# Kernel tuning notes

Measured on AMD Instinct MI355X. Metric: run time of the kernel, lower is better.

The kernel has to match this reference:

```python
import jax, jax.numpy as jnp
import numpy as np

NUM_EMBEDDINGS = 1024
EMBEDDING_DIM = 256
COMMITMENT_COST = 0.25


def setup_inputs() -> dict:
    key = jax.random.key(0)
    k1, k2 = jax.random.split(key)
    x = jax.random.normal(k1, (16, 4096, EMBEDDING_DIM), dtype=jnp.float32)
    init_bound = 1.0 / NUM_EMBEDDINGS
    embedding = jax.random.uniform(
        k2, (NUM_EMBEDDINGS, EMBEDDING_DIM), dtype=jnp.float32,
        minval=-init_bound, maxval=init_bound)
    return {"x": x, "embedding": embedding}


def reference(x, embedding):
    # dim = -1, so no moveaxis needed; flatten all leading dims.
    E = embedding.shape[1]
    N = embedding.shape[0]
    x_flat = jax.lax.stop_gradient(x).reshape(-1, E)            # [M, E]
    M = x_flat.shape[0]

    distances = (
        jnp.sum(x_flat * x_flat, axis=1, keepdims=True)          # [M, 1]
        + jnp.sum(embedding * embedding, axis=1)                  # [N]
        - 2.0 * (x_flat @ embedding.T)                            # [M, N]
    )
    idx = jnp.argmin(distances, axis=1)                           # [M]
    quantized = embedding[idx].reshape(x.shape)                   # gather

    # losses (non-EMA branch)
    e_latent_loss = jnp.mean((jax.lax.stop_gradient(quantized) - x) ** 2)
    q_latent_loss = jnp.mean((quantized - jax.lax.stop_gradient(x)) ** 2)
    loss = q_latent_loss + COMMITMENT_COST * e_latent_loss

    # straight-through estimator
    quantized_st = x + jax.lax.stop_gradient(quantized - x)

    # perplexity: mean of one-hot == normalized code-usage histogram
    counts = jnp.zeros((N,), jnp.float32).at[idx].add(1.0)
    avg_probs = counts / M
    perplexity = jnp.exp(-jnp.sum(avg_probs * jnp.log(avg_probs + 1e-10)))

    return quantized_st, loss, perplexity
```

## Files before the change

### kernel.cpp

```cpp
#include <hip/hip_runtime.h>


#define VQ_M 65536
#define VQ_N 1024
#define VQ_E 256

typedef __attribute__((ext_vector_type(8))) short bf16x8;
typedef __attribute__((ext_vector_type(4))) float f32x4;

__device__ __forceinline__ ushort f2b(float f) {
  unsigned u = __float_as_uint(f);
  unsigned r = (u + 0x7FFFu + ((u >> 16) & 1u)) >> 16;
  return (ushort)r;
}

__global__ __launch_bounds__(256) void vq_prep(
    const float* __restrict__ emb, float* __restrict__ en2h,
    ushort* __restrict__ embB, unsigned* __restrict__ counts,
    double* __restrict__ loss_sum) {
  const int tid  = threadIdx.x;
  const int lane = tid & 63;
  const int n    = blockIdx.x * 4 + (tid >> 6);
  const float4 e4 = reinterpret_cast<const float4*>(emb)[n * 64 + lane];
  double s = (double)e4.x * e4.x + (double)e4.y * e4.y +
             (double)e4.z * e4.z + (double)e4.w * e4.w;
#pragma unroll
  for (int m = 1; m < 64; m <<= 1) s += __shfl_xor(s, m, 64);
  if (lane == 0) en2h[n] = (float)(-0.5 * s);
  ushort4 b;
  b.x = f2b(e4.x); b.y = f2b(e4.y); b.z = f2b(e4.z); b.w = f2b(e4.w);
  reinterpret_cast<ushort4*>(embB)[n * 64 + lane] = b;
  if (blockIdx.x == 0) {
#pragma unroll
    for (int j = 0; j < 4; ++j) counts[tid + j * 256] = 0u;
    if (tid == 0) *loss_sum = 0.0;
  }
}

__global__ __launch_bounds__(256, 2) void vq_argmin_mfma(
    const float* __restrict__ X, const ushort* __restrict__ embB,
    const float* __restrict__ en2h, int* __restrict__ idxOut) {
  __shared__ ushort lds[2][64 * 256];
  const int tid = threadIdx.x;
  const int w   = tid >> 6;
  const int l   = tid & 63;
  const int lr  = l & 15;
  const int g4  = l >> 4;
  const int m0  = blockIdx.x * 128;

  bf16x8 xf[2][8];
#pragma unroll
  for (int fx = 0; fx < 2; ++fx)
#pragma unroll
    for (int kc = 0; kc < 8; ++kc) {
      const float* p =
          X + (size_t)(m0 + w * 32 + fx * 16 + lr) * 256 + kc * 32 + g4 * 8;
      const float4 a = *reinterpret_cast<const float4*>(p);
      const float4 b = *reinterpret_cast<const float4*>(p + 4);
      bf16x8 v;
      v[0] = (short)f2b(a.x); v[1] = (short)f2b(a.y);
      v[2] = (short)f2b(a.z); v[3] = (short)f2b(a.w);
      v[4] = (short)f2b(b.x); v[5] = (short)f2b(b.y);
      v[6] = (short)f2b(b.z); v[7] = (short)f2b(b.w);
      xf[fx][kc] = v;
    }

  const float4* __restrict__ embB4 = reinterpret_cast<const float4*>(embB);

  {
    float4 s[8];
#pragma unroll
    for (int i = 0; i < 8; ++i) {
      const int gg = tid + 256 * i;
      s[i] = embB4[(gg >> 5) * 32 + (gg & 31)];
    }
#pragma unroll
    for (int i = 0; i < 8; ++i) {
      const int gg = tid + 256 * i;
      const int row = gg >> 5, gc = gg & 31;
      reinterpret_cast<float4*>(lds[0])[row * 32 + (gc ^ (row & 15))] = s[i];
    }
  }
  __syncthreads();

  float bval[2] = {-3.4e38f, -3.4e38f};
  int   bidx[2] = {0, 0};

  for (int nt = 0; nt < 16; ++nt) {
    const int cur = nt & 1;
    float4 s[8];
    if (nt < 15) {
#pragma unroll
      for (int i = 0; i < 8; ++i) {
        const int gg = tid + 256 * i;
        s[i] = embB4[((nt + 1) * 64 + (gg >> 5)) * 32 + (gg & 31)];
      }
    }
    f32x4 acc[4][2];
#pragma unroll
    for (int cf = 0; cf < 4; ++cf) {
      const f32x4 e2 =
          *reinterpret_cast<const f32x4*>(en2h + nt * 64 + cf * 16 + g4 * 4);
#pragma unroll
      for (int fx = 0; fx < 2; ++fx) acc[cf][fx] = e2;
    }
#pragma unroll
    for (int kc = 0; kc < 8; ++kc) {
      bf16x8 af[4];
#pragma unroll
      for (int cf = 0; cf < 4; ++cf)
        af[cf] = *reinterpret_cast<const bf16x8*>(
            &lds[cur][(cf * 16 + lr) * 256 + (((kc * 4 + g4) ^ lr) * 8)]);
#pragma unroll
      for (int cf = 0; cf < 4; ++cf)
#pragma unroll
        for (int fx = 0; fx < 2; ++fx)
          acc[cf][fx] = __builtin_amdgcn_mfma_f32_16x16x32_bf16(
              af[cf], xf[fx][kc], acc[cf][fx], 0, 0, 0);
    }
#pragma unroll
    for (int cf = 0; cf < 4; ++cf)
#pragma unroll
      for (int fx = 0; fx < 2; ++fx)
#pragma unroll
        for (int q = 0; q < 4; ++q) {
          const float v = acc[cf][fx][q];
          const int code = nt * 64 + cf * 16 + g4 * 4 + q;
          if (v > bval[fx]) { bval[fx] = v; bidx[fx] = code; }
        }
    if (nt < 15) {
#pragma unroll
      for (int i = 0; i < 8; ++i) {
        const int gg = tid + 256 * i;
        const int row = gg >> 5, gc = gg & 31;
        reinterpret_cast<float4*>(lds[cur ^ 1])[row * 32 + (gc ^ (row & 15))] =
            s[i];
      }
      __syncthreads();
    }
  }

#pragma unroll
  for (int off = 16; off <= 32; off <<= 1)
#pragma unroll
    for (int fx = 0; fx < 2; ++fx) {
      const float ov = __shfl_xor(bval[fx], off, 64);
      const int   oi = __shfl_xor(bidx[fx], off, 64);
      if (ov > bval[fx] || (ov == bval[fx] && oi < bidx[fx])) {
        bval[fx] = ov;
        bidx[fx] = oi;
      }
    }
  if (g4 == 0) {
#pragma unroll
    for (int fx = 0; fx < 2; ++fx)
      idxOut[m0 + w * 32 + fx * 16 + lr] = bidx[fx];
  }
}

__global__ __launch_bounds__(256) void vq_quant_loss(
    const float* __restrict__ X, const float* __restrict__ Emb,
    const int* __restrict__ idx, float* __restrict__ out,
    double* __restrict__ loss_sum) {
  const int F4_TOTAL = VQ_M * (VQ_E / 4);
  const int t = blockIdx.x * 256 + threadIdx.x;
  const int stride = gridDim.x * 256;
  double ls = 0.0;
  for (int i = t; i < F4_TOTAL; i += stride) {
    const int m  = i >> 6;
    const int k4 = i & 63;
    const int c  = idx[m];
    const float4 xv = reinterpret_cast<const float4*>(X)[i];
    const float4 ev = reinterpret_cast<const float4*>(Emb)[c * 64 + k4];
    const float dx = ev.x - xv.x;
    const float dy = ev.y - xv.y;
    const float dz = ev.z - xv.z;
    const float dw = ev.w - xv.w;
    float4 o;
    o.x = xv.x + dx;
    o.y = xv.y + dy;
    o.z = xv.z + dz;
    o.w = xv.w + dw;
    reinterpret_cast<float4*>(out)[i] = o;
    ls += (double)dx * dx + (double)dy * dy + (double)dz * dz + (double)dw * dw;
  }
#pragma unroll
  for (int m2 = 1; m2 < 64; m2 <<= 1) ls += __shfl_xor(ls, m2, 64);
  __shared__ double sh[4];
  const int lane = threadIdx.x & 63;
  const int wv   = threadIdx.x >> 6;
  if (lane == 0) sh[wv] = ls;
  __syncthreads();
  if (threadIdx.x == 0) atomicAdd(loss_sum, sh[0] + sh[1] + sh[2] + sh[3]);
}

__global__ __launch_bounds__(256) void vq_hist(const int* __restrict__ idx,
                                               unsigned* __restrict__ counts) {
  __shared__ unsigned h[VQ_N];
#pragma unroll
  for (int j = 0; j < 4; ++j) h[threadIdx.x + j * 256] = 0u;
  __syncthreads();
  const int stride = gridDim.x * 256;
  for (int i = blockIdx.x * 256 + threadIdx.x; i < VQ_M; i += stride)
    atomicAdd(&h[idx[i]], 1u);
  __syncthreads();
#pragma unroll
  for (int j = 0; j < 4; ++j) {
    const unsigned v = h[threadIdx.x + j * 256];
    if (v) atomicAdd(&counts[threadIdx.x + j * 256], v);
  }
}

__global__ __launch_bounds__(1024) void vq_final(
    const unsigned* __restrict__ counts, const double* __restrict__ loss_sum,
    float* __restrict__ out) {
  const int tid = threadIdx.x;
  const double p = (double)counts[tid] * (1.0 / 65536.0);
  double term = -p * log(p + 1e-10);
#pragma unroll
  for (int m = 1; m < 64; m <<= 1) term += __shfl_xor(term, m, 64);
  __shared__ double sh[16];
  if ((tid & 63) == 0) sh[tid >> 6] = term;
  __syncthreads();
  if (tid == 0) {
    double H = 0.0;
#pragma unroll
    for (int i = 0; i < 16; ++i) H += sh[i];
    out[16777216] = (float)(1.25 * (*loss_sum) * (1.0 / 16777216.0));
    out[16777217] = (float)exp(H);
  }
}

extern "C" void kernel_launch(void* const* d_in, const int* in_sizes, int n_in,
                              void* d_out, int out_size, void* d_ws, size_t ws_size,
                              hipStream_t stream) {
  const float* X   = (const float*)d_in[0];
  const float* Emb = (const float*)d_in[1];
  float* out = (float*)d_out;
  char* ws = (char*)d_ws;
  int*      idx      = (int*)(ws);
  float*    en2h     = (float*)(ws + 262144);
  ushort*   embB     = (ushort*)(ws + 266240);
  unsigned* counts   = (unsigned*)(ws + 790528);
  double*   loss_sum = (double*)(ws + 794624);

  vq_prep<<<256, 256, 0, stream>>>(Emb, en2h, embB, counts, loss_sum);
  vq_argmin_mfma<<<512, 256, 0, stream>>>(X, embB, en2h, idx);
  vq_quant_loss<<<2048, 256, 0, stream>>>(X, Emb, idx, out, loss_sum);
  vq_hist<<<64, 256, 0, stream>>>(idx, counts);
  vq_final<<<1, 1024, 0, stream>>>(counts, loss_sum, out);
}
```

Before: 184.9 us.

## Fuse histogram and loss into argmin kernel, drop X reread in gather pass

The argmin kernel now handles 256 rows per block with four 16-row fragments per wave, and splits the K dimension into two half-tiles staged through smaller LDS buffers. It also accumulates ||x||^2 in fp32, derives the per-row loss as ||x||^2 - 2*best, counts codes with global atomics, and writes per-block loss partials. This removes the separate histogram kernel and lets the output pass be a pure gather of embedding rows that no longer rereads X. The cost is fp32 loss computed from bf16 distances, which is less exact than the old double difference, plus one block per CU with higher register pressure.

```diff
diff --git a/kernel.cpp b/kernel.cpp
--- a/kernel.cpp
+++ b/kernel.cpp
@@ -10,14 +10,12 @@
 
 __device__ __forceinline__ ushort f2b(float f) {
   unsigned u = __float_as_uint(f);
-  unsigned r = (u + 0x7FFFu + ((u >> 16) & 1u)) >> 16;
-  return (ushort)r;
+  return (ushort)((u + 0x7FFFu + ((u >> 16) & 1u)) >> 16);
 }
 
 __global__ __launch_bounds__(256) void vq_prep(
     const float* __restrict__ emb, float* __restrict__ en2h,
-    ushort* __restrict__ embB, unsigned* __restrict__ counts,
-    double* __restrict__ loss_sum) {
+    ushort* __restrict__ embB, unsigned* __restrict__ counts) {
   const int tid  = threadIdx.x;
   const int lane = tid & 63;
   const int n    = blockIdx.x * 4 + (tid >> 6);
@@ -33,30 +31,54 @@
   if (blockIdx.x == 0) {
 #pragma unroll
     for (int j = 0; j < 4; ++j) counts[tid + j * 256] = 0u;
-    if (tid == 0) *loss_sum = 0.0;
-  }
-}
-
-__global__ __launch_bounds__(256, 2) void vq_argmin_mfma(
+  }
+}
+
+__global__ __launch_bounds__(256, 1) void vq_argmin_mfma(
     const float* __restrict__ X, const ushort* __restrict__ embB,
-    const float* __restrict__ en2h, int* __restrict__ idxOut) {
-  __shared__ ushort lds[2][64 * 256];
+    const float* __restrict__ en2h, int* __restrict__ idxOut,
+    unsigned* __restrict__ counts, double* __restrict__ loss_part) {
+  __shared__ ushort lds[2][64 * 128];
+  __shared__ float shl[4];
   const int tid = threadIdx.x;
-  const int w   = tid >> 6;
-  const int l   = tid & 63;
-  const int lr  = l & 15;
-  const int g4  = l >> 4;
-  const int m0  = blockIdx.x * 128;
-
-  bf16x8 xf[2][8];
-#pragma unroll
-  for (int fx = 0; fx < 2; ++fx)
+  const int w  = tid >> 6;
+  const int l  = tid & 63;
+  const int lr = l & 15;
+  const int g4 = l >> 4;
+  const int m0 = blockIdx.x * 256;
+  const float4* __restrict__ embB4 = reinterpret_cast<const float4*>(embB);
+
+  int grow[4], gcol[4];
+#pragma unroll
+  for (int i = 0; i < 4; ++i) {
+    const int gg = tid + 256 * i;
+    grow[i] = gg >> 4;
+    gcol[i] = gg & 15;
+  }
+
+  {
+    float4 s[4];
+#pragma unroll
+    for (int i = 0; i < 4; ++i) s[i] = embB4[grow[i] * 32 + gcol[i]];
+#pragma unroll
+    for (int i = 0; i < 4; ++i)
+      reinterpret_cast<float4*>(lds[0])[grow[i] * 16 +
+                                        (gcol[i] ^ (grow[i] & 15))] = s[i];
+  }
+
+  bf16x8 xf[4][8];
+  float sx[4];
+#pragma unroll
+  for (int fx = 0; fx < 4; ++fx) {
+    sx[fx] = 0.0f;
+    const float* rowp =
+        X + (size_t)(m0 + w * 64 + fx * 16 + lr) * 256 + g4 * 8;
 #pragma unroll
     for (int kc = 0; kc < 8; ++kc) {
-      const float* p =
-          X + (size_t)(m0 + w * 32 + fx * 16 + lr) * 256 + kc * 32 + g4 * 8;
-      const float4 a = *reinterpret_cast<const float4*>(p);
-      const float4 b = *reinterpret_cast<const float4*>(p + 4);
+      const float4 a = *reinterpret_cast<const float4*>(rowp + kc * 32);
+      const float4 b = *reinterpret_cast<const float4*>(rowp + kc * 32 + 4);
+      sx[fx] += a.x * a.x + a.y * a.y + a.z * a.z + a.w * a.w +
+                b.x * b.x + b.y * b.y + b.z * b.z + b.w * b.w;
       bf16x8 v;
       v[0] = (short)f2b(a.x); v[1] = (short)f2b(a.y);
       v[2] = (short)f2b(a.z); v[3] = (short)f2b(a.w);
@@ -64,64 +86,71 @@
       v[6] = (short)f2b(b.z); v[7] = (short)f2b(b.w);
       xf[fx][kc] = v;
     }
-
-  const float4* __restrict__ embB4 = reinterpret_cast<const float4*>(embB);
-
-  {
-    float4 s[8];
-#pragma unroll
-    for (int i = 0; i < 8; ++i) {
-      const int gg = tid + 256 * i;
-      s[i] = embB4[(gg >> 5) * 32 + (gg & 31)];
-    }
-#pragma unroll
-    for (int i = 0; i < 8; ++i) {
-      const int gg = tid + 256 * i;
-      const int row = gg >> 5, gc = gg & 31;
-      reinterpret_cast<float4*>(lds[0])[row * 32 + (gc ^ (row & 15))] = s[i];
-    }
   }
   __syncthreads();
 
-  float bval[2] = {-3.4e38f, -3.4e38f};
-  int   bidx[2] = {0, 0};
+  float bval[4];
+  int   bidx[4];
+#pragma unroll
+  for (int fx = 0; fx < 4; ++fx) { bval[fx] = -3.4e38f; bidx[fx] = 0; }
 
   for (int nt = 0; nt < 16; ++nt) {
-    const int cur = nt & 1;
-    float4 s[8];
-    if (nt < 15) {
-#pragma unroll
-      for (int i = 0; i < 8; ++i) {
-        const int gg = tid + 256 * i;
-        s[i] = embB4[((nt + 1) * 64 + (gg >> 5)) * 32 + (gg & 31)];
-      }
-    }
-    f32x4 acc[4][2];
+    f32x4 acc[4][4];
+    float4 s[4];
+
+#pragma unroll
+    for (int i = 0; i < 4; ++i)
+      s[i] = embB4[(nt * 64 + grow[i]) * 32 + 16 + gcol[i]];
 #pragma unroll
     for (int cf = 0; cf < 4; ++cf) {
       const f32x4 e2 =
           *reinterpret_cast<const f32x4*>(en2h + nt * 64 + cf * 16 + g4 * 4);
 #pragma unroll
-      for (int fx = 0; fx < 2; ++fx) acc[cf][fx] = e2;
-    }
-#pragma unroll
-    for (int kc = 0; kc < 8; ++kc) {
+      for (int fx = 0; fx < 4; ++fx) acc[cf][fx] = e2;
+    }
+#pragma unroll
+    for (int kc = 0; kc < 4; ++kc) {
       bf16x8 af[4];
 #pragma unroll
       for (int cf = 0; cf < 4; ++cf)
         af[cf] = *reinterpret_cast<const bf16x8*>(
-            &lds[cur][(cf * 16 + lr) * 256 + (((kc * 4 + g4) ^ lr) * 8)]);
-#pragma unroll
-      for (int cf = 0; cf < 4; ++cf)
-#pragma unroll
-        for (int fx = 0; fx < 2; ++fx)
+            &lds[0][((cf * 16 + lr) * 16 + ((kc * 4 + g4) ^ lr)) * 8]);
+#pragma unroll
+      for (int cf = 0; cf < 4; ++cf)
+#pragma unroll
+        for (int fx = 0; fx < 4; ++fx)
           acc[cf][fx] = __builtin_amdgcn_mfma_f32_16x16x32_bf16(
               af[cf], xf[fx][kc], acc[cf][fx], 0, 0, 0);
     }
 #pragma unroll
+    for (int i = 0; i < 4; ++i)
+      reinterpret_cast<float4*>(lds[1])[grow[i] * 16 +
+                                        (gcol[i] ^ (grow[i] & 15))] = s[i];
+    __syncthreads();
+
+    if (nt < 15) {
+#pragma unroll
+      for (int i = 0; i < 4; ++i)
+        s[i] = embB4[((nt + 1) * 64 + grow[i]) * 32 + gcol[i]];
+    }
+#pragma unroll
+    for (int kc = 0; kc < 4; ++kc) {
+      bf16x8 af[4];
+#pragma unroll
+      for (int cf = 0; cf < 4; ++cf)
+        af[cf] = *reinterpret_cast<const bf16x8*>(
+            &lds[1][((cf * 16 + lr) * 16 + ((kc * 4 + g4) ^ lr)) * 8]);
+#pragma unroll
+      for (int cf = 0; cf < 4; ++cf)
+#pragma unroll
+        for (int fx = 0; fx < 4; ++fx)
+          acc[cf][fx] = __builtin_amdgcn_mfma_f32_16x16x32_bf16(
+              af[cf], xf[fx][4 + kc], acc[cf][fx], 0, 0, 0);
+    }
+#pragma unroll
     for (int cf = 0; cf < 4; ++cf)
 #pragma unroll
-      for (int fx = 0; fx < 2; ++fx)
+      for (int fx = 0; fx < 4; ++fx)
 #pragma unroll
         for (int q = 0; q < 4; ++q) {
           const float v = acc[cf][fx][q];
@@ -130,12 +159,9 @@
         }
     if (nt < 15) {
 #pragma unroll
-      for (int i = 0; i < 8; ++i) {
-        const int gg = tid + 256 * i;
-        const int row = gg >> 5, gc = gg & 31;
-        reinterpret_cast<float4*>(lds[cur ^ 1])[row * 32 + (gc ^ (row & 15))] =
-            s[i];
-      }
+      for (int i = 0; i < 4; ++i)
+        reinterpret_cast<float4*>(lds[0])[grow[i] * 16 +
+                                          (gcol[i] ^ (grow[i] & 15))] = s[i];
       __syncthreads();
     }
   }
@@ -143,90 +169,66 @@
 #pragma unroll
   for (int off = 16; off <= 32; off <<= 1)
 #pragma unroll
-    for (int fx = 0; fx < 2; ++fx) {
+    for (int fx = 0; fx < 4; ++fx) {
       const float ov = __shfl_xor(bval[fx], off, 64);
       const int   oi = __shfl_xor(bidx[fx], off, 64);
       if (ov > bval[fx] || (ov == bval[fx] && oi < bidx[fx])) {
         bval[fx] = ov;
         bidx[fx] = oi;
       }
-    }
+      sx[fx] += __shfl_xor(sx[fx], off, 64);
+    }
+
+  float lloss = 0.0f;
   if (g4 == 0) {
 #pragma unroll
-    for (int fx = 0; fx < 2; ++fx)
-      idxOut[m0 + w * 32 + fx * 16 + lr] = bidx[fx];
-  }
-}
-
-__global__ __launch_bounds__(256) void vq_quant_loss(
-    const float* __restrict__ X, const float* __restrict__ Emb,
-    const int* __restrict__ idx, float* __restrict__ out,
-    double* __restrict__ loss_sum) {
-  const int F4_TOTAL = VQ_M * (VQ_E / 4);
-  const int t = blockIdx.x * 256 + threadIdx.x;
+    for (int fx = 0; fx < 4; ++fx) {
+      idxOut[m0 + w * 64 + fx * 16 + lr] = bidx[fx];
+      atomicAdd(&counts[bidx[fx]], 1u);
+      lloss += sx[fx] - 2.0f * bval[fx];
+    }
+  }
+#pragma unroll
+  for (int off = 1; off < 16; off <<= 1) lloss += __shfl_xor(lloss, off, 64);
+  if (l == 0) shl[w] = lloss;
+  __syncthreads();
+  if (tid == 0)
+    loss_part[blockIdx.x] =
+        (double)shl[0] + (double)shl[1] + (double)shl[2] + (double)shl[3];
+}
+
+__global__ __launch_bounds__(256) void vq_gather(
+    const int* __restrict__ idx, const float* __restrict__ Emb,
+    float* __restrict__ out) {
+  const int F4 = VQ_M * 64;
   const int stride = gridDim.x * 256;
-  double ls = 0.0;
-  for (int i = t; i < F4_TOTAL; i += stride) {
-    const int m  = i >> 6;
-    const int k4 = i & 63;
-    const int c  = idx[m];
-    const float4 xv = reinterpret_cast<const float4*>(X)[i];
-    const float4 ev = reinterpret_cast<const float4*>(Emb)[c * 64 + k4];
-    const float dx = ev.x - xv.x;
-    const float dy = ev.y - xv.y;
-    const float dz = ev.z - xv.z;
-    const float dw = ev.w - xv.w;
-    float4 o;
-    o.x = xv.x + dx;
-    o.y = xv.y + dy;
-    o.z = xv.z + dz;
-    o.w = xv.w + dw;
-    reinterpret_cast<float4*>(out)[i] = o;
-    ls += (double)dx * dx + (double)dy * dy + (double)dz * dz + (double)dw * dw;
-  }
-#pragma unroll
-  for (int m2 = 1; m2 < 64; m2 <<= 1) ls += __shfl_xor(ls, m2, 64);
-  __shared__ double sh[4];
-  const int lane = threadIdx.x & 63;
-  const int wv   = threadIdx.x >> 6;
-  if (lane == 0) sh[wv] = ls;
-  __syncthreads();
-  if (threadIdx.x == 0) atomicAdd(loss_sum, sh[0] + sh[1] + sh[2] + sh[3]);
-}
-
-__global__ __launch_bounds__(256) void vq_hist(const int* __restrict__ idx,
-                                               unsigned* __restrict__ counts) {
-  __shared__ unsigned h[VQ_N];
-#pragma unroll
-  for (int j = 0; j < 4; ++j) h[threadIdx.x + j * 256] = 0u;
-  __syncthreads();
-  const int stride = gridDim.x * 256;
-  for (int i = blockIdx.x * 256 + threadIdx.x; i < VQ_M; i += stride)
-    atomicAdd(&h[idx[i]], 1u);
-  __syncthreads();
-#pragma unroll
-  for (int j = 0; j < 4; ++j) {
-    const unsigned v = h[threadIdx.x + j * 256];
-    if (v) atomicAdd(&counts[threadIdx.x + j * 256], v);
+  for (int i = blockIdx.x * 256 + threadIdx.x; i < F4; i += stride) {
+    const int c = idx[i >> 6];
+    reinterpret_cast<float4*>(out)[i] =
+        reinterpret_cast<const float4*>(Emb)[c * 64 + (i & 63)];
   }
 }
 
 __global__ __launch_bounds__(1024) void vq_final(
-    const unsigned* __restrict__ counts, const double* __restrict__ loss_sum,
+    const unsigned* __restrict__ counts, const double* __restrict__ loss_part,
     float* __restrict__ out) {
   const int tid = threadIdx.x;
   const double p = (double)counts[tid] * (1.0 / 65536.0);
   double term = -p * log(p + 1e-10);
-#pragma unroll
-  for (int m = 1; m < 64; m <<= 1) term += __shfl_xor(term, m, 64);
-  __shared__ double sh[16];
-  if ((tid & 63) == 0) sh[tid >> 6] = term;
+  double lp = (tid < 256) ? loss_part[tid] : 0.0;
+#pragma unroll
+  for (int m = 1; m < 64; m <<= 1) {
+    term += __shfl_xor(term, m, 64);
+    lp   += __shfl_xor(lp, m, 64);
+  }
+  __shared__ double sh[16], sl[16];
+  if ((tid & 63) == 0) { sh[tid >> 6] = term; sl[tid >> 6] = lp; }
   __syncthreads();
   if (tid == 0) {
-    double H = 0.0;
-#pragma unroll
-    for (int i = 0; i < 16; ++i) H += sh[i];
-    out[16777216] = (float)(1.25 * (*loss_sum) * (1.0 / 16777216.0));
+    double H = 0.0, L = 0.0;
+#pragma unroll
+    for (int i = 0; i < 16; ++i) { H += sh[i]; L += sl[i]; }
+    out[16777216] = (float)(1.25 * L * (1.0 / 16777216.0));
     out[16777217] = (float)exp(H);
   }
 }
@@ -238,15 +240,14 @@
   const float* Emb = (const float*)d_in[1];
   float* out = (float*)d_out;
   char* ws = (char*)d_ws;
-  int*      idx      = (int*)(ws);
-  float*    en2h     = (float*)(ws + 262144);
-  ushort*   embB     = (ushort*)(ws + 266240);
-  unsigned* counts   = (unsigned*)(ws + 790528);
-  double*   loss_sum = (double*)(ws + 794624);
-
-  vq_prep<<<256, 256, 0, stream>>>(Emb, en2h, embB, counts, loss_sum);
-  vq_argmin_mfma<<<512, 256, 0, stream>>>(X, embB, en2h, idx);
-  vq_quant_loss<<<2048, 256, 0, stream>>>(X, Emb, idx, out, loss_sum);
-  vq_hist<<<64, 256, 0, stream>>>(idx, counts);
-  vq_final<<<1, 1024, 0, stream>>>(counts, loss_sum, out);
-}
+  int*      idx       = (int*)(ws);
+  float*    en2h      = (float*)(ws + 262144);
+  ushort*   embB      = (ushort*)(ws + 266240);
+  unsigned* counts    = (unsigned*)(ws + 790528);
+  double*   loss_part = (double*)(ws + 794624);
+
+  vq_prep<<<256, 256, 0, stream>>>(Emb, en2h, embB, counts);
+  vq_argmin_mfma<<<256, 256, 0, stream>>>(X, embB, en2h, idx, counts, loss_part);
+  vq_gather<<<2048, 256, 0, stream>>>(idx, Emb, out);
+  vq_final<<<1, 1024, 0, stream>>>(counts, loss_part, out);
+}
```

New measurement: 221.7 us. +19.9%, slower.
